# Performance work log

Measured on AMD Instinct MI355X. Metric: run time of the kernel, lower is better.

The kernel has to match this reference:

```python
import jax, jax.numpy as jnp
import numpy as np

NEI = 15  # module hard-codes 15 neighbors per node via reshape(N, 15, 2)


def setup_inputs() -> dict:
    N = 10000
    # 15-regular symmetric circulant graph: offsets +-1..+-7 and +N/2 (its own inverse).
    offsets = np.array(list(range(1, 8)) + list(range(-7, 0)) + [N // 2], dtype=np.int64)
    cols = (np.arange(N)[:, None] + offsets[None, :]) % N  # (N, 15)
    adj = np.zeros((N, N), dtype=np.float32)
    adj[np.repeat(np.arange(N), NEI), cols.ravel()] = 1.0
    return {"adjacency_matrix": jnp.asarray(adj)}


def reference(adjacency_matrix):
    N = adjacency_matrix.shape[0]
    # Exactly 15 nonzeros per row -> static size N*15; row-major order matches
    # torch .nonzero(), so reshape gives per-row neighbor columns.
    _, cols = jnp.nonzero(adjacency_matrix, size=N * NEI)
    nb1 = cols.reshape(N, NEI)            # (N,15)   neighbors_one_indexes
    nb2 = nb1[nb1]                        # (N,15,15)  neighbors_two_indexes
    nb3 = nb1[nb2]                        # (N,15,15,15) neighbors_three_indexes
    # closed 3-walk: l-th neighbor of k equals the start node i
    closed = nb3 == jnp.arange(N)[:, None, None, None]
    i, j, k, l = jnp.nonzero(closed)      # data-dependent count (eager)
    # triangles_indexes_test[:, :3] == (i, nb1[i,j], nb2[i,j,k]); temp_l is dropped
    tri = jnp.stack((i, nb1[i, j], nb2[i, j, k]), axis=1)
    tri_sorted = jnp.sort(tri, axis=-1)
    triangles_ids_igraph = jnp.unique(tri_sorted, axis=0)
    return triangles_ids_igraph
```

## Files before the change

kernel.cpp:

```cpp
#include <hip/hip_runtime.h>
#include <math.h>

#define NEI 15
#define ROWSTRIDE 16

typedef float f4 __attribute__((ext_vector_type(4)));

#define GET16(n0, n1, n2, n3, K)                                   \
    ((K) < 8                                                       \
         ? ((K) < 4                                                \
                ? ((K) == 0 ? (n0).x : (K) == 1 ? (n0).y           \
                                : (K) == 2 ? (n0).z : (n0).w)      \
                : ((K) == 4 ? (n1).x : (K) == 5 ? (n1).y           \
                                : (K) == 6 ? (n1).z : (n1).w))     \
         : ((K) < 12                                               \
                ? ((K) == 8 ? (n2).x : (K) == 9 ? (n2).y           \
                                : (K) == 10 ? (n2).z : (n2).w)     \
                : ((K) == 12 ? (n3).x : (K) == 13 ? (n3).y         \
                                : (K) == 14 ? (n3).z : (n3).w)))

__device__ __forceinline__ int mbcnt64(unsigned long long m) {
    int c = __builtin_amdgcn_mbcnt_lo((unsigned)m, 0);
    c = __builtin_amdgcn_mbcnt_hi((unsigned)(m >> 32), c);
    return c;
}

__global__ void find_nb_kernel(const float* __restrict__ A,
                               int* __restrict__ nb, int N, int totalWaves) {
    const int wavesPerBlock = blockDim.x >> 6;
    const int waveId = blockIdx.x * wavesPerBlock + (threadIdx.x >> 6);
    const int lane = threadIdx.x & 63;
    const int n4 = N >> 2;

    for (int row = waveId; row < N; row += totalWaves) {
        const f4* rowp = reinterpret_cast<const f4*>(A + (long long)row * N);
        int count = 0;

        for (int c0 = 0; c0 < n4; c0 += 256) {
            const int i0 = c0 + lane;
            const int i1 = i0 + 64, i2 = i0 + 128, i3 = i0 + 192;
            f4 v0 = {0.f, 0.f, 0.f, 0.f}, v1 = {0.f, 0.f, 0.f, 0.f};
            f4 v2 = {0.f, 0.f, 0.f, 0.f}, v3 = {0.f, 0.f, 0.f, 0.f};
            if (i0 < n4) v0 = __builtin_nontemporal_load(&rowp[i0]);
            if (i1 < n4) v1 = __builtin_nontemporal_load(&rowp[i1]);
            if (i2 < n4) v2 = __builtin_nontemporal_load(&rowp[i2]);
            if (i3 < n4) v3 = __builtin_nontemporal_load(&rowp[i3]);

            const bool a0 = (v0.x != 0.f) || (v0.y != 0.f) || (v0.z != 0.f) || (v0.w != 0.f);
            const bool a1 = (v1.x != 0.f) || (v1.y != 0.f) || (v1.z != 0.f) || (v1.w != 0.f);
            const bool a2 = (v2.x != 0.f) || (v2.y != 0.f) || (v2.z != 0.f) || (v2.w != 0.f);
            const bool a3 = (v3.x != 0.f) || (v3.y != 0.f) || (v3.z != 0.f) || (v3.w != 0.f);
            if (__ballot(a0 || a1 || a2 || a3) == 0ull) continue;

            #pragma unroll
            for (int q = 0; q < 4; ++q) {
                const f4 v = (q == 0) ? v0 : (q == 1) ? v1 : (q == 2) ? v2 : v3;
                const int idx = c0 + q * 64 + lane;
                const unsigned long long m0 = __ballot(v.x != 0.f);
                const unsigned long long m1 = __ballot(v.y != 0.f);
                const unsigned long long m2 = __ballot(v.z != 0.f);
                const unsigned long long m3 = __ballot(v.w != 0.f);
                if ((m0 | m1 | m2 | m3) != 0ull) {
                    const int below = mbcnt64(m0) + mbcnt64(m1) + mbcnt64(m2) + mbcnt64(m3);
                    const int b0 = (int)((m0 >> lane) & 1ull);
                    const int b1 = (int)((m1 >> lane) & 1ull);
                    const int b2 = (int)((m2 >> lane) & 1ull);
                    const int base = count + below;
                    if (v.x != 0.f) { const int p = base;                if (p < NEI) nb[row * ROWSTRIDE + p] = (idx << 2) + 0; }
                    if (v.y != 0.f) { const int p = base + b0;           if (p < NEI) nb[row * ROWSTRIDE + p] = (idx << 2) + 1; }
                    if (v.z != 0.f) { const int p = base + b0 + b1;      if (p < NEI) nb[row * ROWSTRIDE + p] = (idx << 2) + 2; }
                    if (v.w != 0.f) { const int p = base + b0 + b1 + b2; if (p < NEI) nb[row * ROWSTRIDE + p] = (idx << 2) + 3; }
                    count += __popcll(m0) + __popcll(m1) + __popcll(m2) + __popcll(m3);
                }
            }
        }
        const int base4 = n4 << 2;
        const int rem = N - base4;
        if (rem > 0) {
            float v = 0.f;
            if (lane < rem) v = A[(long long)row * N + base4 + lane];
            const unsigned long long m = __ballot(v != 0.f);
            if (v != 0.f) {
                const int p = count + mbcnt64(m);
                if (p < NEI) nb[row * ROWSTRIDE + p] = base4 + lane;
            }
        }
    }
}

__global__ void count_tri_kernel(const int* __restrict__ nb,
                                 int* __restrict__ mask2,
                                 int* __restrict__ offs2,
                                 int* __restrict__ blockSums, int N) {
    __shared__ int partial[256];
    const int tid = blockIdx.x * 256 + threadIdx.x;
    const int M = N * NEI;
    int c = 0, mask = 0;
    if (tid < M) {
        const int i = tid / NEI;
        const int j = tid - i * NEI;
        const int a = nb[i * ROWSTRIDE + j];
        if (a > i) {
            const int4* np = reinterpret_cast<const int4*>(nb + a * ROWSTRIDE);
            const int4 n0 = np[0], n1 = np[1], n2 = np[2], n3 = np[3];
            const int4* vp = reinterpret_cast<const int4*>(nb + i * ROWSTRIDE);
            const int4 w0 = vp[0], w1 = vp[1], w2 = vp[2], w3 = vp[3];
            #pragma unroll
            for (int k = 1; k < NEI; ++k) {
                if (k > j) {
                    const int b = GET16(w0, w1, w2, w3, k);
                    const bool adj =
                        (n0.x == b) || (n0.y == b) || (n0.z == b) || (n0.w == b) ||
                        (n1.x == b) || (n1.y == b) || (n1.z == b) || (n1.w == b) ||
                        (n2.x == b) || (n2.y == b) || (n2.z == b) || (n2.w == b) ||
                        (n3.x == b) || (n3.y == b) || (n3.z == b);
                    if (adj) { mask |= (1 << k); ++c; }
                }
            }
        }
        mask2[tid] = mask;
    }
    partial[threadIdx.x] = c;
    __syncthreads();
    #pragma unroll
    for (int d = 1; d < 256; d <<= 1) {
        const int mine  = partial[threadIdx.x];
        const int other = (threadIdx.x >= d) ? partial[threadIdx.x - d] : 0;
        __syncthreads();
        partial[threadIdx.x] = mine + other;
        __syncthreads();
    }
    if (tid < M) offs2[tid] = (threadIdx.x == 0) ? 0 : partial[threadIdx.x - 1];
    if (threadIdx.x == 255) blockSums[blockIdx.x] = partial[255];
}

__global__ __launch_bounds__(256) void emit_tri_kernel(const int* __restrict__ nb,
                                                       const int* __restrict__ mask2,
                                                       const int* __restrict__ offs2,
                                                       const int* __restrict__ blockSums,
                                                       int* __restrict__ out, int N) {
    __shared__ int red[256];
    const int tid = blockIdx.x * 256 + threadIdx.x;
    const int M = N * NEI;

    int s = 0;
    for (int idx = threadIdx.x; idx < blockIdx.x; idx += 256) s += blockSums[idx];
    red[threadIdx.x] = s;
    __syncthreads();
    #pragma unroll
    for (int d = 128; d >= 1; d >>= 1) {
        if (threadIdx.x < d) red[threadIdx.x] += red[threadIdx.x + d];
        __syncthreads();
    }
    const int blockOff = red[0];

    if (tid >= M) return;
    const int mask = mask2[tid];
    if (mask == 0) return;
    const int i = tid / NEI;
    const int j = tid - i * NEI;
    const int a = nb[i * ROWSTRIDE + j];
    const int4* vp = reinterpret_cast<const int4*>(nb + i * ROWSTRIDE);
    const int4 w0 = vp[0], w1 = vp[1], w2 = vp[2], w3 = vp[3];
    int pos = blockOff + offs2[tid];
    #pragma unroll
    for (int k = 1; k < NEI; ++k) {
        if ((mask >> k) & 1) {
            const int b = GET16(w0, w1, w2, w3, k);
            out[3 * pos + 0] = i;
            out[3 * pos + 1] = a;
            out[3 * pos + 2] = b;
            ++pos;
        }
    }
}

extern "C" void kernel_launch(void* const* d_in, const int* in_sizes, int n_in,
                              void* d_out, int out_size, void* d_ws, size_t ws_size,
                              hipStream_t stream) {
    const float* A = (const float*)d_in[0];
    const long long total = (long long)in_sizes[0];
    const int N = (int)llround(sqrt((double)total));
    const int M = N * NEI;
    const int B = (M + 255) / 256;

    int* ws = (int*)d_ws;
    int* w_nb    = ws;
    int* w_mask2 = ws + N * ROWSTRIDE;
    int* w_offs2 = w_mask2 + M;
    int* w_bsum  = w_offs2 + M;

    int* out = (int*)d_out;

    {
        int totalWaves = (N <= 8192) ? N : (N + 1) / 2;
        const int blocks = (totalWaves + 3) / 4;
        totalWaves = blocks * 4;
        find_nb_kernel<<<blocks, 256, 0, stream>>>(A, w_nb, N, totalWaves);
    }
    count_tri_kernel<<<B, 256, 0, stream>>>(w_nb, w_mask2, w_offs2, w_bsum, N);
    emit_tri_kernel<<<B, 256, 0, stream>>>(w_nb, w_mask2, w_offs2, w_bsum, out, N);
}
```

Baseline: 75.36 us.

## Fuse triangle count and emit kernels with a grid-wide arrival barrier

Replaces the separate count and emit kernels with one persistent-style kernel. Each block scans its counts, publishes a block sum, spins on an atomic arrival counter until every block has arrived, then computes its offset and writes triangles directly from registers. This drops one kernel launch and the global round trip for the mask and offset arrays. It relies on all blocks (at most 1024 here, about 586 for N=10000) being co-resident; otherwise the spin barrier deadlocks.

```diff
diff --git a/kernel.cpp b/kernel.cpp
--- a/kernel.cpp
+++ b/kernel.cpp
@@ -3,6 +3,7 @@
 
 #define NEI 15
 #define ROWSTRIDE 16
+#define MAXB_FUSED 1024
 
 typedef float f4 __attribute__((ext_vector_type(4)));
 
@@ -26,7 +27,10 @@
 }
 
 __global__ void find_nb_kernel(const float* __restrict__ A,
-                               int* __restrict__ nb, int N, int totalWaves) {
+                               int* __restrict__ nb,
+                               int* __restrict__ arrivals,
+                               int N, int totalWaves) {
+    if (blockIdx.x == 0 && threadIdx.x == 0) *arrivals = 0;
     const int wavesPerBlock = blockDim.x >> 6;
     const int waveId = blockIdx.x * wavesPerBlock + (threadIdx.x >> 6);
     const int lane = threadIdx.x & 63;
@@ -83,6 +87,89 @@
             if (v != 0.f) {
                 const int p = count + mbcnt64(m);
                 if (p < NEI) nb[row * ROWSTRIDE + p] = base4 + lane;
+            }
+        }
+    }
+}
+
+__global__ __launch_bounds__(256, 4) void tri_fused_kernel(
+        const int* __restrict__ nb,
+        int* blockSums, int* arrivals,
+        int* __restrict__ out, int N, int B) {
+    __shared__ int partial[256];
+    const int tid = blockIdx.x * 256 + threadIdx.x;
+    const int M = N * NEI;
+
+    int c = 0, mask = 0, i = 0, j = 0, a = 0;
+    int4 w0 = {0,0,0,0}, w1 = {0,0,0,0}, w2 = {0,0,0,0}, w3 = {0,0,0,0};
+    if (tid < M) {
+        i = tid / NEI;
+        j = tid - i * NEI;
+        a = nb[i * ROWSTRIDE + j];
+        if (a > i) {
+            const int4* np = reinterpret_cast<const int4*>(nb + a * ROWSTRIDE);
+            const int4 n0 = np[0], n1 = np[1], n2 = np[2], n3 = np[3];
+            const int4* vp = reinterpret_cast<const int4*>(nb + i * ROWSTRIDE);
+            w0 = vp[0]; w1 = vp[1]; w2 = vp[2]; w3 = vp[3];
+            #pragma unroll
+            for (int k = 1; k < NEI; ++k) {
+                if (k > j) {
+                    const int b = GET16(w0, w1, w2, w3, k);
+                    const bool adj =
+                        (n0.x == b) || (n0.y == b) || (n0.z == b) || (n0.w == b) ||
+                        (n1.x == b) || (n1.y == b) || (n1.z == b) || (n1.w == b) ||
+                        (n2.x == b) || (n2.y == b) || (n2.z == b) || (n2.w == b) ||
+                        (n3.x == b) || (n3.y == b) || (n3.z == b);
+                    if (adj) { mask |= (1 << k); ++c; }
+                }
+            }
+        }
+    }
+
+    partial[threadIdx.x] = c;
+    __syncthreads();
+    #pragma unroll
+    for (int d = 1; d < 256; d <<= 1) {
+        const int mine  = partial[threadIdx.x];
+        const int other = (threadIdx.x >= d) ? partial[threadIdx.x - d] : 0;
+        __syncthreads();
+        partial[threadIdx.x] = mine + other;
+        __syncthreads();
+    }
+    const int localExcl  = (threadIdx.x == 0) ? 0 : partial[threadIdx.x - 1];
+    const int blockTotal = partial[255];
+
+    if (threadIdx.x == 0) {
+        blockSums[blockIdx.x] = blockTotal;
+        __threadfence();
+        atomicAdd(arrivals, 1);
+        while (__hip_atomic_load(arrivals, __ATOMIC_ACQUIRE,
+                                 __HIP_MEMORY_SCOPE_AGENT) < B)
+            __builtin_amdgcn_s_sleep(16);
+    }
+    __syncthreads();
+
+    int s = 0;
+    for (int idx = threadIdx.x; idx < blockIdx.x; idx += 256) s += blockSums[idx];
+    partial[threadIdx.x] = s;
+    __syncthreads();
+    #pragma unroll
+    for (int d = 128; d >= 1; d >>= 1) {
+        if (threadIdx.x < d) partial[threadIdx.x] += partial[threadIdx.x + d];
+        __syncthreads();
+    }
+    const int blockOff = partial[0];
+
+    if (tid < M && mask != 0) {
+        int pos = blockOff + localExcl;
+        #pragma unroll
+        for (int k = 1; k < NEI; ++k) {
+            if ((mask >> k) & 1) {
+                const int b = GET16(w0, w1, w2, w3, k);
+                out[3 * pos + 0] = i;
+                out[3 * pos + 1] = a;
+                out[3 * pos + 2] = b;
+                ++pos;
             }
         }
     }
@@ -142,7 +229,6 @@
     __shared__ int red[256];
     const int tid = blockIdx.x * 256 + threadIdx.x;
     const int M = N * NEI;
-
     int s = 0;
     for (int idx = threadIdx.x; idx < blockIdx.x; idx += 256) s += blockSums[idx];
     red[threadIdx.x] = s;
@@ -186,9 +272,10 @@
 
     int* ws = (int*)d_ws;
     int* w_nb    = ws;
-    int* w_mask2 = ws + N * ROWSTRIDE;
+    int* w_bsum  = ws + N * ROWSTRIDE;
+    int* w_arr   = w_bsum + B;
+    int* w_mask2 = w_arr + 1;
     int* w_offs2 = w_mask2 + M;
-    int* w_bsum  = w_offs2 + M;
 
     int* out = (int*)d_out;
 
@@ -196,8 +283,12 @@
         int totalWaves = (N <= 8192) ? N : (N + 1) / 2;
         const int blocks = (totalWaves + 3) / 4;
         totalWaves = blocks * 4;
-        find_nb_kernel<<<blocks, 256, 0, stream>>>(A, w_nb, N, totalWaves);
-    }
-    count_tri_kernel<<<B, 256, 0, stream>>>(w_nb, w_mask2, w_offs2, w_bsum, N);
-    emit_tri_kernel<<<B, 256, 0, stream>>>(w_nb, w_mask2, w_offs2, w_bsum, out, N);
-}
+        find_nb_kernel<<<blocks, 256, 0, stream>>>(A, w_nb, w_arr, N, totalWaves);
+    }
+    if (B <= MAXB_FUSED) {
+        tri_fused_kernel<<<B, 256, 0, stream>>>(w_nb, w_bsum, w_arr, out, N, B);
+    } else {
+        count_tri_kernel<<<B, 256, 0, stream>>>(w_nb, w_mask2, w_offs2, w_bsum, N);
+        emit_tri_kernel<<<B, 256, 0, stream>>>(w_nb, w_mask2, w_offs2, w_bsum, out, N);
+    }
+}
```

New measurement: 121.6 us. 1.61x slower.
